# Kernel tuning notes

Hardware: AMD Instinct MI355X
Metric: run time of the kernel (lower is better)

## Reference

```python
import jax, jax.numpy as jnp
import numpy as np

B, N, DM, H = 1, 2048, 1024, 16
CURV = 1.0  # hyperbolic curvature


def setup_inputs() -> dict:
    key = jax.random.key(0)
    ks = jax.random.split(key, 5)
    s = 1.0 / np.sqrt(DM)  # nn.Linear default init scale
    x = jax.random.normal(ks[0], (B, N, DM), dtype=jnp.float32)
    Wq = jax.random.uniform(ks[1], (DM, DM), jnp.float32, -s, s)
    Wk = jax.random.uniform(ks[2], (DM, DM), jnp.float32, -s, s)
    Wv = jax.random.uniform(ks[3], (DM, DM), jnp.float32, -s, s)
    Wo = jax.random.uniform(ks[4], (DM, DM), jnp.float32, -s, s)
    return {"x": x, "Wq": Wq, "Wk": Wk, "Wv": Wv, "Wo": Wo}


def reference(x, Wq, Wk, Wv, Wo):
    b, n, d = x.shape
    hd = d // H

    def split_heads(t):  # [B,N,D] -> [B,H,N,hd]
        return t.reshape(b, n, H, hd).transpose(0, 2, 1, 3)

    q = split_heads(x @ Wq.T)
    k = split_heads(x @ Wk.T)
    v = split_heads(x @ Wv.T)

    q_norm_sq = jnp.sum(q * q, axis=-1, keepdims=True)      # [B,H,N,1]
    k_norm_sq = jnp.sum(k * k, axis=-1)[:, :, None, :]      # [B,H,1,N]
    qk = jnp.einsum('bhnd,bhmd->bhnm', q, k)                # [B,H,N,N]

    diff_sq = jnp.maximum(q_norm_sq + k_norm_sq - 2.0 * qk, 0.0)
    denom = jnp.maximum((1.0 - CURV * q_norm_sq) * (1.0 - CURV * k_norm_sq), 1e-6)
    cosh_arg = jnp.maximum(1.0 + 2.0 * CURV * diff_sq / denom, 1.0)
    # safe acosh: acosh(1)=0; mask avoids inf grad at the boundary
    distance = jnp.where(cosh_arg > 1.0,
                         jnp.arccosh(jnp.maximum(cosh_arg, 1.0 + 1e-12)),
                         0.0)

    attn = jax.nn.softmax(-distance, axis=-1)               # [B,H,N,N]
    out = jnp.einsum('bhnm,bhmd->bhnd', attn, v)            # [B,H,N,hd]
    out = out.transpose(0, 2, 1, 3).reshape(b, n, d)
    return out @ Wo.T
```

## Files before the change

### kernel.cpp

```cpp
#include <hip/hip_runtime.h>
#include <math.h>

#define NSEQ   2048
#define DMODEL 1024
#define NHEADS 16
#define HD     64

typedef short bf16x8 __attribute__((ext_vector_type(8)));
typedef float f32x4  __attribute__((ext_vector_type(4)));
typedef unsigned short ushort8_t __attribute__((ext_vector_type(8)));

__device__ __forceinline__ unsigned short f2bf(float x) {
    unsigned int u = __builtin_bit_cast(unsigned int, x);
    unsigned int r = (u + 0x7FFFu + ((u >> 16) & 1u)) >> 16;
    return (unsigned short)r;
}

__global__ __launch_bounds__(256) void convert_inputs(
    const float* __restrict__ x,  const float* __restrict__ Wq,
    const float* __restrict__ Wk, const float* __restrict__ Wv,
    const float* __restrict__ Wo,
    unsigned short* __restrict__ xb, unsigned short* __restrict__ Wb,
    unsigned short* __restrict__ Wob)
{
    const size_t i8 = ((size_t)blockIdx.x * 256 + threadIdx.x) * 8;
    const float* src;
    unsigned short* dst;
    if (i8 < (2ull << 20)) {
        src = x + i8;  dst = xb + i8;
    } else if (i8 < (5ull << 20)) {
        const size_t o = i8 - (2ull << 20);
        const size_t s = o >> 20;
        src = (s == 0 ? Wq : (s == 1 ? Wk : Wv)) + (o & ((1u << 20) - 1));
        dst = Wb + o;
    } else {
        const size_t o = i8 - (5ull << 20);
        src = Wo + o;  dst = Wob + o;
    }
    const float4 v0 = *reinterpret_cast<const float4*>(src);
    const float4 v1 = *reinterpret_cast<const float4*>(src + 4);
    ushort8_t r;
    r[0] = f2bf(v0.x); r[1] = f2bf(v0.y); r[2] = f2bf(v0.z); r[3] = f2bf(v0.w);
    r[4] = f2bf(v1.x); r[5] = f2bf(v1.y); r[6] = f2bf(v1.z); r[7] = f2bf(v1.w);
    *reinterpret_cast<ushort8_t*>(dst) = r;
}

template <int QKV>
__global__ __launch_bounds__(256) void gemm_bt_bf16(
    const unsigned short* __restrict__ A, const unsigned short* __restrict__ B,
    float* __restrict__ C0,
    unsigned short* __restrict__ QbO, float* __restrict__ qnO,
    float* __restrict__ cq2O,
    unsigned short* __restrict__ KbO, float* __restrict__ knO,
    float* __restrict__ ckO,
    unsigned short* __restrict__ VbO)
{
    __shared__ unsigned short Ahs[128 * 72];
    __shared__ unsigned short Bhs[128 * 72];

    const int bm   = blockIdx.x * 128;
    const int bn   = blockIdx.y * 128;
    const int t    = threadIdx.x;
    const int wid  = t >> 6;
    const int lane = t & 63;
    const int g    = lane >> 4;
    const int r    = lane & 15;
    const int wm   = (wid >> 1) * 64;
    const int wn   = (wid & 1) * 64;

    f32x4 acc[4][4];
#pragma unroll
    for (int i = 0; i < 4; ++i)
#pragma unroll
        for (int j = 0; j < 4; ++j) acc[i][j] = (f32x4){0.f, 0.f, 0.f, 0.f};

    const int srow = t >> 1;
    const int sseg = (t & 1) * 32;

    for (int k0 = 0; k0 < DMODEL; k0 += 64) {
        __syncthreads();
        ushort8_t av[4], bv[4];
#pragma unroll
        for (int c = 0; c < 4; ++c) {
            av[c] = *reinterpret_cast<const ushort8_t*>(
                &A[(size_t)(bm + srow) * DMODEL + k0 + sseg + c * 8]);
            bv[c] = *reinterpret_cast<const ushort8_t*>(
                &B[(size_t)(bn + srow) * DMODEL + k0 + sseg + c * 8]);
        }
#pragma unroll
        for (int c = 0; c < 4; ++c) {
            *reinterpret_cast<ushort8_t*>(&Ahs[srow * 72 + sseg + c * 8]) = av[c];
            *reinterpret_cast<ushort8_t*>(&Bhs[srow * 72 + sseg + c * 8]) = bv[c];
        }
        __syncthreads();

#pragma unroll
        for (int dc = 0; dc < 2; ++dc) {
            bf16x8 af[4], bfr[4];
#pragma unroll
            for (int mt = 0; mt < 4; ++mt)
                af[mt] = *reinterpret_cast<const bf16x8*>(
                    &Ahs[(wm + mt * 16 + r) * 72 + dc * 32 + g * 8]);
#pragma unroll
            for (int nt = 0; nt < 4; ++nt)
                bfr[nt] = *reinterpret_cast<const bf16x8*>(
                    &Bhs[(wn + nt * 16 + r) * 72 + dc * 32 + g * 8]);
#pragma unroll
            for (int mt = 0; mt < 4; ++mt)
#pragma unroll
                for (int nt = 0; nt < 4; ++nt)
                    acc[mt][nt] = __builtin_amdgcn_mfma_f32_16x16x32_bf16(
                        af[mt], bfr[nt], acc[mt][nt], 0, 0, 0);
        }
    }

    if (QKV) {
        const int sel = bn >> 10;
        const int bnl = bn & 1023;
        if (sel < 2) {
            unsigned short* Hb = sel ? KbO : QbO;
            float* narr = sel ? knO : qnO;
            float* carr = sel ? ckO : cq2O;
            const int hh = (bnl + wn) >> 6;
#pragma unroll
            for (int mt = 0; mt < 4; ++mt) {
#pragma unroll
                for (int rg = 0; rg < 4; ++rg) {
                    float ss = 0.f;
#pragma unroll
                    for (int nt = 0; nt < 4; ++nt) {
                        const float v = acc[mt][nt][rg];
                        ss = fmaf(v, v, ss);
                        Hb[(size_t)(bm + wm + mt * 16 + g * 4 + rg) * 1024 +
                           bnl + wn + nt * 16 + r] = f2bf(v);
                    }
                    ss += __shfl_xor(ss, 1, 64);
                    ss += __shfl_xor(ss, 2, 64);
                    ss += __shfl_xor(ss, 4, 64);
                    ss += __shfl_xor(ss, 8, 64);
                    if (r == 0) {
                        const int row = bm + wm + mt * 16 + g * 4 + rg;
                        narr[hh * NSEQ + row] = ss;
                        carr[hh * NSEQ + row] =
                            (sel ? 1.0f : 2.0f) / (1.0f - ss);
                    }
                }
            }
        } else {
#pragma unroll
            for (int mt = 0; mt < 4; ++mt)
#pragma unroll
                for (int nt = 0; nt < 4; ++nt)
#pragma unroll
                    for (int rg = 0; rg < 4; ++rg)
                        VbO[(size_t)(bm + wm + mt * 16 + g * 4 + rg) * 1024 +
                            bnl + wn + nt * 16 + r] = f2bf(acc[mt][nt][rg]);
        }
    } else {
#pragma unroll
        for (int mt = 0; mt < 4; ++mt)
#pragma unroll
            for (int nt = 0; nt < 4; ++nt)
#pragma unroll
                for (int rg = 0; rg < 4; ++rg)
                    C0[(size_t)(bm + wm + mt * 16 + g * 4 + rg) * 1024 +
                       bn + wn + nt * 16 + r] = acc[mt][nt][rg];
    }
}

__global__ __launch_bounds__(256) void vt_kernel_bf16(
    const unsigned short* __restrict__ Vb, unsigned short* __restrict__ Vt)
{
    __shared__ unsigned short Vs[64 * 72];
    const int h   = blockIdx.y;
    const int n0  = blockIdx.x * 64;
    const int t   = threadIdx.x;
    const int row = t >> 2;
    const int seg = (t & 3) * 16;

    const unsigned short* src = Vb + (size_t)(n0 + row) * 1024 + h * HD + seg;
    *reinterpret_cast<ushort8_t*>(&Vs[row * 72 + seg]) =
        *reinterpret_cast<const ushort8_t*>(src);
    *reinterpret_cast<ushort8_t*>(&Vs[row * 72 + seg + 8]) =
        *reinterpret_cast<const ushort8_t*>(src + 8);
    __syncthreads();

    ushort8_t a, b;
#pragma unroll
    for (int c = 0; c < 8; ++c) a[c] = Vs[(seg + c) * 72 + row];
#pragma unroll
    for (int c = 0; c < 8; ++c) b[c] = Vs[(seg + 8 + c) * 72 + row];
    unsigned short* dst = Vt + (size_t)(h * HD + row) * NSEQ + n0 + seg;
    *reinterpret_cast<ushort8_t*>(dst)     = a;
    *reinterpret_cast<ushort8_t*>(dst + 8) = b;
}

__global__ __launch_bounds__(256) void hyp_attn_v3(
    const unsigned short* __restrict__ Qb, const unsigned short* __restrict__ Kb,
    const unsigned short* __restrict__ Vt,
    const float* __restrict__ qn_a, const float* __restrict__ cq2_a,
    const float* __restrict__ kn_a, const float* __restrict__ ck_a,
    float* __restrict__ Opart, float* __restrict__ lpart)
{
    __shared__ unsigned short Khs[64 * 64];
    __shared__ unsigned short Vts[64 * 64];
    __shared__ unsigned short Ps[4][16 * 64];

    const int h    = blockIdx.y;
    const int n0   = blockIdx.x * 64;
    const int jh   = blockIdx.z;
    const int t    = threadIdx.x;
    const int wid  = t >> 6;
    const int lane = t & 63;
    const int g    = lane >> 4;
    const int r    = lane & 15;
    const int qb   = n0 + wid * 16;

    bf16x8 qf[2];
#pragma unroll
    for (int dc = 0; dc < 2; ++dc)
        qf[dc] = *reinterpret_cast<const bf16x8*>(
            Qb + (size_t)(qb + r) * DMODEL + h * HD + dc * 32 + g * 8);

    float qn_r[4], c2q[4];
#pragma unroll
    for (int rg = 0; rg < 4; ++rg) {
        qn_r[rg] = qn_a[h * NSEQ + qb + g * 4 + rg];
        c2q[rg]  = cq2_a[h * NSEQ + qb + g * 4 + rg];
    }

    f32x4 oacc[4];
#pragma unroll
    for (int nt = 0; nt < 4; ++nt) oacc[nt] = (f32x4){0.f, 0.f, 0.f, 0.f};
    float l_acc[4] = {0.f, 0.f, 0.f, 0.f};

    const int srow = t >> 2;
    const int c0   = (t & 3) * 2;
    const int sw0  = (c0 ^ (srow & 7)) * 8;
    const int sw1  = ((c0 + 1) ^ (srow & 7)) * 8;
    const int sg   = (t & 3) * 16;
    unsigned short* Pw = &Ps[wid][0];

    for (int tb = 0; tb < 16; ++tb) {
        const int j0 = jh * 1024 + tb * 64;
        __syncthreads();
        {
            const unsigned short* ks = Kb + (size_t)(j0 + srow) * DMODEL + h * HD + sg;
            const unsigned short* vs = Vt + (size_t)(h * HD + srow) * NSEQ + j0 + sg;
            *reinterpret_cast<ushort8_t*>(&Khs[srow * 64 + sw0]) =
                *reinterpret_cast<const ushort8_t*>(ks);
            *reinterpret_cast<ushort8_t*>(&Khs[srow * 64 + sw1]) =
                *reinterpret_cast<const ushort8_t*>(ks + 8);
            *reinterpret_cast<ushort8_t*>(&Vts[srow * 64 + sw0]) =
                *reinterpret_cast<const ushort8_t*>(vs);
            *reinterpret_cast<ushort8_t*>(&Vts[srow * 64 + sw1]) =
                *reinterpret_cast<const ushort8_t*>(vs + 8);
        }
        __syncthreads();

#pragma unroll
        for (int jt = 0; jt < 4; ++jt) {
            f32x4 sac = (f32x4){0.f, 0.f, 0.f, 0.f};
#pragma unroll
            for (int dc = 0; dc < 2; ++dc) {
                const bf16x8 kb = *reinterpret_cast<const bf16x8*>(
                    &Khs[(jt * 16 + r) * 64 + ((dc * 4 + g) ^ (r & 7)) * 8]);
                sac = __builtin_amdgcn_mfma_f32_16x16x32_bf16(qf[dc], kb, sac, 0, 0, 0);
            }
            const int jj = j0 + jt * 16 + r;
            const float kn_v = kn_a[h * NSEQ + jj];
            const float ck_v = ck_a[h * NSEQ + jj];
#pragma unroll
            for (int rg = 0; rg < 4; ++rg) {
                const float dsq = fmaf(-2.f, sac[rg], qn_r[rg] + kn_v);
                const float ca  = fmaxf(fmaf(dsq, c2q[rg] * ck_v, 1.f), 1.0f);
                const float s2  = fmaf(ca, ca, -1.f);
                const float wj  = ca - __builtin_amdgcn_sqrtf(s2);
                l_acc[rg] += wj;
                const int qrow = g * 4 + rg;
                Pw[qrow * 64 +
                   ((2 * jt + (r >> 3)) ^ (qrow & 7)) * 8 + (r & 7)] = f2bf(wj);
            }
        }

#pragma unroll
        for (int kc = 0; kc < 2; ++kc) {
            const bf16x8 pa = *reinterpret_cast<const bf16x8*>(
                &Pw[r * 64 + ((kc * 4 + g) ^ (r & 7)) * 8]);
#pragma unroll
            for (int nt = 0; nt < 4; ++nt) {
                const bf16x8 vb = *reinterpret_cast<const bf16x8*>(
                    &Vts[(nt * 16 + r) * 64 + ((kc * 4 + g) ^ (r & 7)) * 8]);
                oacc[nt] = __builtin_amdgcn_mfma_f32_16x16x32_bf16(pa, vb, oacc[nt], 0, 0, 0);
            }
        }
    }

#pragma unroll
    for (int rg = 0; rg < 4; ++rg) {
        l_acc[rg] += __shfl_xor(l_acc[rg], 1, 64);
        l_acc[rg] += __shfl_xor(l_acc[rg], 2, 64);
        l_acc[rg] += __shfl_xor(l_acc[rg], 4, 64);
        l_acc[rg] += __shfl_xor(l_acc[rg], 8, 64);
    }

    float* Op = Opart + (size_t)jh * NSEQ * DMODEL;
#pragma unroll
    for (int nt = 0; nt < 4; ++nt)
#pragma unroll
        for (int rg = 0; rg < 4; ++rg)
            Op[(size_t)(qb + g * 4 + rg) * DMODEL + h * HD + nt * 16 + r] =
                oacc[nt][rg];
    if (r == 0) {
#pragma unroll
        for (int rg = 0; rg < 4; ++rg)
            lpart[(jh * NHEADS + h) * NSEQ + qb + g * 4 + rg] = l_acc[rg];
    }
}

__global__ __launch_bounds__(256) void merge_kernel(
    const float* __restrict__ Opart, const float* __restrict__ lpart,
    unsigned short* __restrict__ Ob)
{
    const size_t i8 = ((size_t)blockIdx.x * 256 + threadIdx.x) * 8;
    if (i8 >= (size_t)NSEQ * DMODEL) return;
    const int n  = (int)(i8 >> 10);
    const int dm = (int)(i8 & 1023);
    const int h  = dm >> 6;
    const float li = 1.0f / (lpart[h * NSEQ + n] +
                             lpart[(NHEADS + h) * NSEQ + n]);
    const float* O0 = Opart + i8;
    const float* O1 = Opart + (size_t)NSEQ * DMODEL + i8;
    ushort8_t o;
#pragma unroll
    for (int c = 0; c < 2; ++c) {
        const float4 a = *reinterpret_cast<const float4*>(O0 + c * 4);
        const float4 b = *reinterpret_cast<const float4*>(O1 + c * 4);
        o[c * 4 + 0] = f2bf((a.x + b.x) * li);
        o[c * 4 + 1] = f2bf((a.y + b.y) * li);
        o[c * 4 + 2] = f2bf((a.z + b.z) * li);
        o[c * 4 + 3] = f2bf((a.w + b.w) * li);
    }
    *reinterpret_cast<ushort8_t*>(Ob + i8) = o;
}

extern "C" void kernel_launch(void* const* d_in, const int* in_sizes, int n_in,
                              void* d_out, int out_size, void* d_ws, size_t ws_size,
                              hipStream_t stream)
{
    const float* x  = (const float*)d_in[0];
    const float* Wq = (const float*)d_in[1];
    const float* Wk = (const float*)d_in[2];
    const float* Wv = (const float*)d_in[3];
    const float* Wo = (const float*)d_in[4];
    float* out = (float*)d_out;

    char* ws = (char*)d_ws;
    const size_t MB = 1048576;
    unsigned short* xb   = (unsigned short*)(ws);
    unsigned short* Wb   = (unsigned short*)(ws + 4  * MB);
    unsigned short* Wob  = (unsigned short*)(ws + 10 * MB);
    unsigned short* Qbuf = (unsigned short*)(ws + 12 * MB);
    unsigned short* Kbuf = (unsigned short*)(ws + 16 * MB);
    unsigned short* Vb   = (unsigned short*)(ws + 20 * MB);
    unsigned short* Vt   = (unsigned short*)(ws + 24 * MB);
    float*          qn   = (float*)(ws + 28 * MB);
    float*          cq2  = qn  + NHEADS * NSEQ;
    float*          kn   = cq2 + NHEADS * NSEQ;
    float*          ck   = kn  + NHEADS * NSEQ;
    float*          Opart= (float*)(ws + 29 * MB);
    float*          lpart= (float*)(ws + 45 * MB);
    unsigned short* Ob   = xb;

    const dim3 blk(256);

    convert_inputs<<<3072, blk, 0, stream>>>(x, Wq, Wk, Wv, Wo, xb, Wb, Wob);

    gemm_bt_bf16<1><<<dim3(NSEQ / 128, 3072 / 128), blk, 0, stream>>>(
        xb, Wb, nullptr, Qbuf, qn, cq2, Kbuf, kn, ck, Vb);

    vt_kernel_bf16<<<dim3(NSEQ / 64, NHEADS), blk, 0, stream>>>(Vb, Vt);

    hyp_attn_v3<<<dim3(NSEQ / 64, NHEADS, 2), blk, 0, stream>>>(
        Qbuf, Kbuf, Vt, qn, cq2, kn, ck, Opart, lpart);

    merge_kernel<<<(NSEQ * DMODEL / 8 + 255) / 256, blk, 0, stream>>>(
        Opart, lpart, Ob);

    gemm_bt_bf16<0><<<dim3(NSEQ / 128, DMODEL / 128), blk, 0, stream>>>(
        Ob, Wob, out, nullptr, nullptr, nullptr,
        nullptr, nullptr, nullptr, nullptr);
}
```

Measured before the change: 112.3 us.

## Fuse split-KV merge into output GEMM and transpose score MFMA for packed P stores

Removes the separate merge kernel by having the output projection GEMM read both fp32 partial attention outputs, sum and normalize them by the combined row sums, and convert to bf16 while staging its A tile. The attention kernel swaps the MFMA operands so each lane holds four consecutive keys for one query row. This allows vectorized float4 loads of key norms and packed bf16 stores of P through v_cvt_pk_bf16_f32, and cuts the row-sum reduction to two shuffles. The costs are that the output GEMM now reads fp32 partials (double the bytes) with no load pipelining, and the merge work is repeated across the 8 column blocks.

```diff
diff --git a/kernel.cpp b/kernel.cpp
--- a/kernel.cpp
+++ b/kernel.cpp
@@ -14,6 +14,11 @@
     unsigned int u = __builtin_bit_cast(unsigned int, x);
     unsigned int r = (u + 0x7FFFu + ((u >> 16) & 1u)) >> 16;
     return (unsigned short)r;
+}
+__device__ __forceinline__ unsigned int cvt_pk_bf16(float lo, float hi) {
+    unsigned int d;
+    asm("v_cvt_pk_bf16_f32 %0, %1, %2" : "=v"(d) : "v"(lo), "v"(hi));
+    return d;
 }
 
 __global__ __launch_bounds__(256) void convert_inputs(
@@ -45,10 +50,8 @@
     *reinterpret_cast<ushort8_t*>(dst) = r;
 }
 
-template <int QKV>
-__global__ __launch_bounds__(256) void gemm_bt_bf16(
+__global__ __launch_bounds__(256) void gemm_qkv(
     const unsigned short* __restrict__ A, const unsigned short* __restrict__ B,
-    float* __restrict__ C0,
     unsigned short* __restrict__ QbO, float* __restrict__ qnO,
     float* __restrict__ cq2O,
     unsigned short* __restrict__ KbO, float* __restrict__ knO,
@@ -114,47 +117,35 @@
         }
     }
 
-    if (QKV) {
-        const int sel = bn >> 10;
-        const int bnl = bn & 1023;
-        if (sel < 2) {
-            unsigned short* Hb = sel ? KbO : QbO;
-            float* narr = sel ? knO : qnO;
-            float* carr = sel ? ckO : cq2O;
-            const int hh = (bnl + wn) >> 6;
-#pragma unroll
-            for (int mt = 0; mt < 4; ++mt) {
-#pragma unroll
-                for (int rg = 0; rg < 4; ++rg) {
-                    float ss = 0.f;
-#pragma unroll
-                    for (int nt = 0; nt < 4; ++nt) {
-                        const float v = acc[mt][nt][rg];
-                        ss = fmaf(v, v, ss);
-                        Hb[(size_t)(bm + wm + mt * 16 + g * 4 + rg) * 1024 +
-                           bnl + wn + nt * 16 + r] = f2bf(v);
-                    }
-                    ss += __shfl_xor(ss, 1, 64);
-                    ss += __shfl_xor(ss, 2, 64);
-                    ss += __shfl_xor(ss, 4, 64);
-                    ss += __shfl_xor(ss, 8, 64);
-                    if (r == 0) {
-                        const int row = bm + wm + mt * 16 + g * 4 + rg;
-                        narr[hh * NSEQ + row] = ss;
-                        carr[hh * NSEQ + row] =
-                            (sel ? 1.0f : 2.0f) / (1.0f - ss);
-                    }
+    const int sel = bn >> 10;
+    const int bnl = bn & 1023;
+    if (sel < 2) {
+        unsigned short* Hb = sel ? KbO : QbO;
+        float* narr = sel ? knO : qnO;
+        float* carr = sel ? ckO : cq2O;
+        const int hh = (bnl + wn) >> 6;
+#pragma unroll
+        for (int mt = 0; mt < 4; ++mt) {
+#pragma unroll
+            for (int rg = 0; rg < 4; ++rg) {
+                float ss = 0.f;
+#pragma unroll
+                for (int nt = 0; nt < 4; ++nt) {
+                    const float v = acc[mt][nt][rg];
+                    ss = fmaf(v, v, ss);
+                    Hb[(size_t)(bm + wm + mt * 16 + g * 4 + rg) * 1024 +
+                       bnl + wn + nt * 16 + r] = f2bf(v);
+                }
+                ss += __shfl_xor(ss, 1, 64);
+                ss += __shfl_xor(ss, 2, 64);
+                ss += __shfl_xor(ss, 4, 64);
+                ss += __shfl_xor(ss, 8, 64);
+                if (r == 0) {
+                    const int row = bm + wm + mt * 16 + g * 4 + rg;
+                    narr[hh * NSEQ + row] = ss;
+                    carr[hh * NSEQ + row] = (sel ? 1.0f : 2.0f) / (1.0f - ss);
                 }
             }
-        } else {
-#pragma unroll
-            for (int mt = 0; mt < 4; ++mt)
-#pragma unroll
-                for (int nt = 0; nt < 4; ++nt)
-#pragma unroll
-                    for (int rg = 0; rg < 4; ++rg)
-                        VbO[(size_t)(bm + wm + mt * 16 + g * 4 + rg) * 1024 +
-                            bnl + wn + nt * 16 + r] = f2bf(acc[mt][nt][rg]);
         }
     } else {
 #pragma unroll
@@ -163,8 +154,8 @@
             for (int nt = 0; nt < 4; ++nt)
 #pragma unroll
                 for (int rg = 0; rg < 4; ++rg)
-                    C0[(size_t)(bm + wm + mt * 16 + g * 4 + rg) * 1024 +
-                       bn + wn + nt * 16 + r] = acc[mt][nt][rg];
+                    VbO[(size_t)(bm + wm + mt * 16 + g * 4 + rg) * 1024 +
+                        bnl + wn + nt * 16 + r] = f2bf(acc[mt][nt][rg]);
     }
 }
 
@@ -195,7 +186,7 @@
     *reinterpret_cast<ushort8_t*>(dst + 8) = b;
 }
 
-__global__ __launch_bounds__(256) void hyp_attn_v3(
+__global__ __launch_bounds__(256) void hyp_attn_v4(
     const unsigned short* __restrict__ Qb, const unsigned short* __restrict__ Kb,
     const unsigned short* __restrict__ Vt,
     const float* __restrict__ qn_a, const float* __restrict__ cq2_a,
@@ -222,17 +213,13 @@
         qf[dc] = *reinterpret_cast<const bf16x8*>(
             Qb + (size_t)(qb + r) * DMODEL + h * HD + dc * 32 + g * 8);
 
-    float qn_r[4], c2q[4];
-#pragma unroll
-    for (int rg = 0; rg < 4; ++rg) {
-        qn_r[rg] = qn_a[h * NSEQ + qb + g * 4 + rg];
-        c2q[rg]  = cq2_a[h * NSEQ + qb + g * 4 + rg];
-    }
+    const float qn_l = qn_a[h * NSEQ + qb + r];
+    const float c2q  = cq2_a[h * NSEQ + qb + r];
 
     f32x4 oacc[4];
 #pragma unroll
     for (int nt = 0; nt < 4; ++nt) oacc[nt] = (f32x4){0.f, 0.f, 0.f, 0.f};
-    float l_acc[4] = {0.f, 0.f, 0.f, 0.f};
+    float l_acc = 0.f;
 
     const int srow = t >> 2;
     const int c0   = (t & 3) * 2;
@@ -240,6 +227,7 @@
     const int sw1  = ((c0 + 1) ^ (srow & 7)) * 8;
     const int sg   = (t & 3) * 16;
     unsigned short* Pw = &Ps[wid][0];
+    char* PwB = (char*)Pw + r * 128 + 8 * (g & 1);
 
     for (int tb = 0; tb < 16; ++tb) {
         const int j0 = jh * 1024 + tb * 64;
@@ -265,22 +253,30 @@
             for (int dc = 0; dc < 2; ++dc) {
                 const bf16x8 kb = *reinterpret_cast<const bf16x8*>(
                     &Khs[(jt * 16 + r) * 64 + ((dc * 4 + g) ^ (r & 7)) * 8]);
-                sac = __builtin_amdgcn_mfma_f32_16x16x32_bf16(qf[dc], kb, sac, 0, 0, 0);
+                sac = __builtin_amdgcn_mfma_f32_16x16x32_bf16(kb, qf[dc], sac, 0, 0, 0);
             }
-            const int jj = j0 + jt * 16 + r;
-            const float kn_v = kn_a[h * NSEQ + jj];
-            const float ck_v = ck_a[h * NSEQ + jj];
+            const int jbase = j0 + jt * 16 + g * 4;
+            const float4 kn4 = *reinterpret_cast<const float4*>(
+                &kn_a[h * NSEQ + jbase]);
+            const float4 ck4 = *reinterpret_cast<const float4*>(
+                &ck_a[h * NSEQ + jbase]);
+            const float knv[4] = {kn4.x, kn4.y, kn4.z, kn4.w};
+            const float ckv[4] = {ck4.x, ck4.y, ck4.z, ck4.w};
+            float w[4];
 #pragma unroll
             for (int rg = 0; rg < 4; ++rg) {
-                const float dsq = fmaf(-2.f, sac[rg], qn_r[rg] + kn_v);
-                const float ca  = fmaxf(fmaf(dsq, c2q[rg] * ck_v, 1.f), 1.0f);
+                const float dsq = fmaf(-2.f, sac[rg], qn_l + knv[rg]);
+                const float ca  = fmaxf(fmaf(dsq, c2q * ckv[rg], 1.f), 1.0f);
                 const float s2  = fmaf(ca, ca, -1.f);
                 const float wj  = ca - __builtin_amdgcn_sqrtf(s2);
-                l_acc[rg] += wj;
-                const int qrow = g * 4 + rg;
-                Pw[qrow * 64 +
-                   ((2 * jt + (r >> 3)) ^ (qrow & 7)) * 8 + (r & 7)] = f2bf(wj);
+                l_acc += wj;
+                w[rg] = wj;
             }
+            uint2 pkd;
+            pkd.x = cvt_pk_bf16(w[0], w[1]);
+            pkd.y = cvt_pk_bf16(w[2], w[3]);
+            *reinterpret_cast<uint2*>(
+                PwB + (((2 * jt + (g >> 1)) ^ (r & 7)) << 4)) = pkd;
         }
 
 #pragma unroll
@@ -296,13 +292,8 @@
         }
     }
 
-#pragma unroll
-    for (int rg = 0; rg < 4; ++rg) {
-        l_acc[rg] += __shfl_xor(l_acc[rg], 1, 64);
-        l_acc[rg] += __shfl_xor(l_acc[rg], 2, 64);
-        l_acc[rg] += __shfl_xor(l_acc[rg], 4, 64);
-        l_acc[rg] += __shfl_xor(l_acc[rg], 8, 64);
-    }
+    l_acc += __shfl_xor(l_acc, 16, 64);
+    l_acc += __shfl_xor(l_acc, 32, 64);
 
     float* Op = Opart + (size_t)jh * NSEQ * DMODEL;
 #pragma unroll
@@ -311,37 +302,97 @@
         for (int rg = 0; rg < 4; ++rg)
             Op[(size_t)(qb + g * 4 + rg) * DMODEL + h * HD + nt * 16 + r] =
                 oacc[nt][rg];
-    if (r == 0) {
-#pragma unroll
-        for (int rg = 0; rg < 4; ++rg)
-            lpart[(jh * NHEADS + h) * NSEQ + qb + g * 4 + rg] = l_acc[rg];
+    if (lane < 16)
+        lpart[(jh * NHEADS + h) * NSEQ + qb + r] = l_acc;
+}
+
+__global__ __launch_bounds__(256) void gemm_out_merge(
+    const float* __restrict__ O0, const float* __restrict__ O1,
+    const float* __restrict__ lp,
+    const unsigned short* __restrict__ B,
+    float* __restrict__ C)
+{
+    __shared__ unsigned short Ahs[128 * 72];
+    __shared__ unsigned short Bhs[128 * 72];
+
+    const int bm   = blockIdx.x * 128;
+    const int bn   = blockIdx.y * 128;
+    const int t    = threadIdx.x;
+    const int wid  = t >> 6;
+    const int lane = t & 63;
+    const int g    = lane >> 4;
+    const int r    = lane & 15;
+    const int wm   = (wid >> 1) * 64;
+    const int wn   = (wid & 1) * 64;
+
+    f32x4 acc[4][4];
+#pragma unroll
+    for (int i = 0; i < 4; ++i)
+#pragma unroll
+        for (int j = 0; j < 4; ++j) acc[i][j] = (f32x4){0.f, 0.f, 0.f, 0.f};
+
+    const int srow = t >> 1;
+    const int sseg = (t & 1) * 32;
+    const int arow = bm + srow;
+
+    for (int k0 = 0; k0 < DMODEL; k0 += 64) {
+        __syncthreads();
+        const int hseg = (k0 + sseg) >> 6;
+        const float li = __builtin_amdgcn_rcpf(
+            lp[hseg * NSEQ + arow] + lp[(NHEADS + hseg) * NSEQ + arow]);
+        const float* a0 = &O0[(size_t)arow * DMODEL + k0 + sseg];
+        const float* a1 = &O1[(size_t)arow * DMODEL + k0 + sseg];
+        unsigned int pk8[16];
+#pragma unroll
+        for (int c = 0; c < 8; ++c) {
+            const float4 x0 = *reinterpret_cast<const float4*>(a0 + c * 4);
+            const float4 y0 = *reinterpret_cast<const float4*>(a1 + c * 4);
+            pk8[2 * c]     = cvt_pk_bf16((x0.x + y0.x) * li, (x0.y + y0.y) * li);
+            pk8[2 * c + 1] = cvt_pk_bf16((x0.z + y0.z) * li, (x0.w + y0.w) * li);
+        }
+        ushort8_t bv[4];
+#pragma unroll
+        for (int c = 0; c < 4; ++c)
+            bv[c] = *reinterpret_cast<const ushort8_t*>(
+                &B[(size_t)(bn + srow) * DMODEL + k0 + sseg + c * 8]);
+#pragma unroll
+        for (int c = 0; c < 4; ++c) {
+            uint4 w;
+            w.x = pk8[4 * c]; w.y = pk8[4 * c + 1];
+            w.z = pk8[4 * c + 2]; w.w = pk8[4 * c + 3];
+            *reinterpret_cast<uint4*>(&Ahs[srow * 72 + sseg + c * 8]) = w;
+            *reinterpret_cast<ushort8_t*>(&Bhs[srow * 72 + sseg + c * 8]) = bv[c];
+        }
+        __syncthreads();
+
+#pragma unroll
+        for (int dc = 0; dc < 2; ++dc) {
+            bf16x8 af[4], bfr[4];
+#pragma unroll
+            for (int mt = 0; mt < 4; ++mt)
+                af[mt] = *reinterpret_cast<const bf16x8*>(
+                    &Ahs[(wm + mt * 16 + r) * 72 + dc * 32 + g * 8]);
+#pragma unroll
+            for (int nt = 0; nt < 4; ++nt)
+                bfr[nt] = *reinterpret_cast<const bf16x8*>(
+                    &Bhs[(wn + nt * 16 + r) * 72 + dc * 32 + g * 8]);
+#pragma unroll
+            for (int mt = 0; mt < 4; ++mt)
+#pragma unroll
+                for (int nt = 0; nt < 4; ++nt)
+                    acc[mt][nt] = __builtin_amdgcn_mfma_f32_16x16x32_bf16(
+                        af[mt], bfr[nt], acc[mt][nt], 0, 0, 0);
+        }
     }
-}
-
-__global__ __launch_bounds__(256) void merge_kernel(
-    const float* __restrict__ Opart, const float* __restrict__ lpart,
-    unsigned short* __restrict__ Ob)
-{
-    const size_t i8 = ((size_t)blockIdx.x * 256 + threadIdx.x) * 8;
-    if (i8 >= (size_t)NSEQ * DMODEL) return;
-    const int n  = (int)(i8 >> 10);
-    const int dm = (int)(i8 & 1023);
-    const int h  = dm >> 6;
-    const float li = 1.0f / (lpart[h * NSEQ + n] +
-                             lpart[(NHEADS + h) * NSEQ + n]);
-    const float* O0 = Opart + i8;
-    const float* O1 = Opart + (size_t)NSEQ * DMODEL + i8;
-    ushort8_t o;
-#pragma unroll
-    for (int c = 0; c < 2; ++c) {
-        const float4 a = *reinterpret_cast<const float4*>(O0 + c * 4);
-        const float4 b = *reinterpret_cast<const float4*>(O1 + c * 4);
-        o[c * 4 + 0] = f2bf((a.x + b.x) * li);
-        o[c * 4 + 1] = f2bf((a.y + b.y) * li);
-        o[c * 4 + 2] = f2bf((a.z + b.z) * li);
-        o[c * 4 + 3] = f2bf((a.w + b.w) * li);
-    }
-    *reinterpret_cast<ushort8_t*>(Ob + i8) = o;
+
+#pragma unroll
+    for (int mt = 0; mt < 4; ++mt)
+#pragma unroll
+        for (int nt = 0; nt < 4; ++nt)
+#pragma unroll
+            for (int rg = 0; rg < 4; ++rg)
+                C[(size_t)(bm + wm + mt * 16 + g * 4 + rg) * 1024 +
+                  bn + wn + nt * 16 + r] = acc[mt][nt][rg];
 }
 
 extern "C" void kernel_launch(void* const* d_in, const int* in_sizes, int n_in,
@@ -370,24 +421,19 @@
     float*          ck   = kn  + NHEADS * NSEQ;
     float*          Opart= (float*)(ws + 29 * MB);
     float*          lpart= (float*)(ws + 45 * MB);
-    unsigned short* Ob   = xb;
 
     const dim3 blk(256);
 
     convert_inputs<<<3072, blk, 0, stream>>>(x, Wq, Wk, Wv, Wo, xb, Wb, Wob);
 
-    gemm_bt_bf16<1><<<dim3(NSEQ / 128, 3072 / 128), blk, 0, stream>>>(
-        xb, Wb, nullptr, Qbuf, qn, cq2, Kbuf, kn, ck, Vb);
+    gemm_qkv<<<dim3(NSEQ / 128, 3072 / 128), blk, 0, stream>>>(
+        xb, Wb, Qbuf, qn, cq2, Kbuf, kn, ck, Vb);
 
     vt_kernel_bf16<<<dim3(NSEQ / 64, NHEADS), blk, 0, stream>>>(Vb, Vt);
 
-    hyp_attn_v3<<<dim3(NSEQ / 64, NHEADS, 2), blk, 0, stream>>>(
+    hyp_attn_v4<<<dim3(NSEQ / 64, NHEADS, 2), blk, 0, stream>>>(
         Qbuf, Kbuf, Vt, qn, cq2, kn, ck, Opart, lpart);
 
-    merge_kernel<<<(NSEQ * DMODEL / 8 + 255) / 256, blk, 0, stream>>>(
-        Opart, lpart, Ob);
-
-    gemm_bt_bf16<0><<<dim3(NSEQ / 128, DMODEL / 128), blk, 0, stream>>>(
-        Ob, Wob, out, nullptr, nullptr, nullptr,
-        nullptr, nullptr, nullptr, nullptr);
-}
+    gemm_out_merge<<<dim3(NSEQ / 128, DMODEL / 128), blk, 0, stream>>>(
+        Opart, Opart + (size_t)NSEQ * DMODEL, lpart, Wob, out);
+}
```

Result: slower. 151.5 us (+34.9%).

## Fuse fp32-to-bf16 conversion into GEMM tile loads with XOR-swizzled LDS

Applied to the files above, without the earlier changes.

Removes the separate input conversion kernel. Both GEMMs now read fp32 x and the weights directly and pack them to bf16 with v_cvt_pk_bf16_f32 while staging tiles into shared memory. The shared-memory tiles also switch from padded rows to an XOR swizzle, which shrinks LDS use while still avoiding bank conflicts. The trade-off is that each GEMM block reads twice the global bytes, and inputs are re-read and re-converted once per tile row and column, instead of once up front.

```diff
diff --git a/kernel.cpp b/kernel.cpp
--- a/kernel.cpp
+++ b/kernel.cpp
@@ -15,48 +15,24 @@
     unsigned int r = (u + 0x7FFFu + ((u >> 16) & 1u)) >> 16;
     return (unsigned short)r;
 }
-
-__global__ __launch_bounds__(256) void convert_inputs(
-    const float* __restrict__ x,  const float* __restrict__ Wq,
-    const float* __restrict__ Wk, const float* __restrict__ Wv,
-    const float* __restrict__ Wo,
-    unsigned short* __restrict__ xb, unsigned short* __restrict__ Wb,
-    unsigned short* __restrict__ Wob)
-{
-    const size_t i8 = ((size_t)blockIdx.x * 256 + threadIdx.x) * 8;
-    const float* src;
-    unsigned short* dst;
-    if (i8 < (2ull << 20)) {
-        src = x + i8;  dst = xb + i8;
-    } else if (i8 < (5ull << 20)) {
-        const size_t o = i8 - (2ull << 20);
-        const size_t s = o >> 20;
-        src = (s == 0 ? Wq : (s == 1 ? Wk : Wv)) + (o & ((1u << 20) - 1));
-        dst = Wb + o;
-    } else {
-        const size_t o = i8 - (5ull << 20);
-        src = Wo + o;  dst = Wob + o;
-    }
-    const float4 v0 = *reinterpret_cast<const float4*>(src);
-    const float4 v1 = *reinterpret_cast<const float4*>(src + 4);
-    ushort8_t r;
-    r[0] = f2bf(v0.x); r[1] = f2bf(v0.y); r[2] = f2bf(v0.z); r[3] = f2bf(v0.w);
-    r[4] = f2bf(v1.x); r[5] = f2bf(v1.y); r[6] = f2bf(v1.z); r[7] = f2bf(v1.w);
-    *reinterpret_cast<ushort8_t*>(dst) = r;
-}
-
-template <int QKV>
-__global__ __launch_bounds__(256) void gemm_bt_bf16(
-    const unsigned short* __restrict__ A, const unsigned short* __restrict__ B,
-    float* __restrict__ C0,
+__device__ __forceinline__ unsigned int cvt_pk_bf16(float lo, float hi) {
+    unsigned int d;
+    asm("v_cvt_pk_bf16_f32 %0, %1, %2" : "=v"(d) : "v"(lo), "v"(hi));
+    return d;
+}
+
+__global__ __launch_bounds__(256) void gemm_qkv(
+    const float* __restrict__ X,
+    const float* __restrict__ Wq, const float* __restrict__ Wk,
+    const float* __restrict__ Wv,
     unsigned short* __restrict__ QbO, float* __restrict__ qnO,
     float* __restrict__ cq2O,
     unsigned short* __restrict__ KbO, float* __restrict__ knO,
     float* __restrict__ ckO,
     unsigned short* __restrict__ VbO)
 {
-    __shared__ unsigned short Ahs[128 * 72];
-    __shared__ unsigned short Bhs[128 * 72];
+    __shared__ unsigned short Ahs[128 * 64];
+    __shared__ unsigned short Bhs[128 * 64];
 
     const int bm   = blockIdx.x * 128;
     const int bn   = blockIdx.y * 128;
@@ -68,6 +44,10 @@
     const int wm   = (wid >> 1) * 64;
     const int wn   = (wid & 1) * 64;
 
+    const int sel = bn >> 10;
+    const int bnl = bn & 1023;
+    const float* Bp = (sel == 0) ? Wq : ((sel == 1) ? Wk : Wv);
+
     f32x4 acc[4][4];
 #pragma unroll
     for (int i = 0; i < 4; ++i)
@@ -75,22 +55,33 @@
         for (int j = 0; j < 4; ++j) acc[i][j] = (f32x4){0.f, 0.f, 0.f, 0.f};
 
     const int srow = t >> 1;
-    const int sseg = (t & 1) * 32;
+    const int shal = (t & 1) * 32;
 
     for (int k0 = 0; k0 < DMODEL; k0 += 64) {
         __syncthreads();
-        ushort8_t av[4], bv[4];
+        const float* ag = &X[(size_t)(bm + srow) * DMODEL + k0 + shal];
+        const float* bg = &Bp[(size_t)(bnl + srow) * DMODEL + k0 + shal];
+        unsigned int apk[16], bpk[16];
+#pragma unroll
+        for (int c4 = 0; c4 < 8; ++c4) {
+            const float4 va = *reinterpret_cast<const float4*>(ag + c4 * 4);
+            apk[2 * c4]     = cvt_pk_bf16(va.x, va.y);
+            apk[2 * c4 + 1] = cvt_pk_bf16(va.z, va.w);
+            const float4 vb = *reinterpret_cast<const float4*>(bg + c4 * 4);
+            bpk[2 * c4]     = cvt_pk_bf16(vb.x, vb.y);
+            bpk[2 * c4 + 1] = cvt_pk_bf16(vb.z, vb.w);
+        }
 #pragma unroll
         for (int c = 0; c < 4; ++c) {
-            av[c] = *reinterpret_cast<const ushort8_t*>(
-                &A[(size_t)(bm + srow) * DMODEL + k0 + sseg + c * 8]);
-            bv[c] = *reinterpret_cast<const ushort8_t*>(
-                &B[(size_t)(bn + srow) * DMODEL + k0 + sseg + c * 8]);
-        }
-#pragma unroll
-        for (int c = 0; c < 4; ++c) {
-            *reinterpret_cast<ushort8_t*>(&Ahs[srow * 72 + sseg + c * 8]) = av[c];
-            *reinterpret_cast<ushort8_t*>(&Bhs[srow * 72 + sseg + c * 8]) = bv[c];
+            const int seg = (t & 1) * 4 + c;
+            const int sw  = (seg ^ (srow & 7)) * 8;
+            uint4 wa, wb;
+            wa.x = apk[4 * c]; wa.y = apk[4 * c + 1];
+            wa.z = apk[4 * c + 2]; wa.w = apk[4 * c + 3];
+            wb.x = bpk[4 * c]; wb.y = bpk[4 * c + 1];
+            wb.z = bpk[4 * c + 2]; wb.w = bpk[4 * c + 3];
+            *reinterpret_cast<uint4*>(&Ahs[srow * 64 + sw]) = wa;
+            *reinterpret_cast<uint4*>(&Bhs[srow * 64 + sw]) = wb;
         }
         __syncthreads();
 
@@ -100,11 +91,11 @@
 #pragma unroll
             for (int mt = 0; mt < 4; ++mt)
                 af[mt] = *reinterpret_cast<const bf16x8*>(
-                    &Ahs[(wm + mt * 16 + r) * 72 + dc * 32 + g * 8]);
+                    &Ahs[(wm + mt * 16 + r) * 64 + ((dc * 4 + g) ^ (r & 7)) * 8]);
 #pragma unroll
             for (int nt = 0; nt < 4; ++nt)
                 bfr[nt] = *reinterpret_cast<const bf16x8*>(
-                    &Bhs[(wn + nt * 16 + r) * 72 + dc * 32 + g * 8]);
+                    &Bhs[(wn + nt * 16 + r) * 64 + ((dc * 4 + g) ^ (r & 7)) * 8]);
 #pragma unroll
             for (int mt = 0; mt < 4; ++mt)
 #pragma unroll
@@ -114,47 +105,33 @@
         }
     }
 
-    if (QKV) {
-        const int sel = bn >> 10;
-        const int bnl = bn & 1023;
-        if (sel < 2) {
-            unsigned short* Hb = sel ? KbO : QbO;
-            float* narr = sel ? knO : qnO;
-            float* carr = sel ? ckO : cq2O;
-            const int hh = (bnl + wn) >> 6;
-#pragma unroll
-            for (int mt = 0; mt < 4; ++mt) {
-#pragma unroll
-                for (int rg = 0; rg < 4; ++rg) {
-                    float ss = 0.f;
-#pragma unroll
-                    for (int nt = 0; nt < 4; ++nt) {
-                        const float v = acc[mt][nt][rg];
-                        ss = fmaf(v, v, ss);
-                        Hb[(size_t)(bm + wm + mt * 16 + g * 4 + rg) * 1024 +
-                           bnl + wn + nt * 16 + r] = f2bf(v);
-                    }
-                    ss += __shfl_xor(ss, 1, 64);
-                    ss += __shfl_xor(ss, 2, 64);
-                    ss += __shfl_xor(ss, 4, 64);
-                    ss += __shfl_xor(ss, 8, 64);
-                    if (r == 0) {
-                        const int row = bm + wm + mt * 16 + g * 4 + rg;
-                        narr[hh * NSEQ + row] = ss;
-                        carr[hh * NSEQ + row] =
-                            (sel ? 1.0f : 2.0f) / (1.0f - ss);
-                    }
+    if (sel < 2) {
+        unsigned short* Hb = sel ? KbO : QbO;
+        float* narr = sel ? knO : qnO;
+        float* carr = sel ? ckO : cq2O;
+        const int hh = (bnl + wn) >> 6;
+#pragma unroll
+        for (int mt = 0; mt < 4; ++mt) {
+#pragma unroll
+            for (int rg = 0; rg < 4; ++rg) {
+                float ss = 0.f;
+#pragma unroll
+                for (int nt = 0; nt < 4; ++nt) {
+                    const float v = acc[mt][nt][rg];
+                    ss = fmaf(v, v, ss);
+                    Hb[(size_t)(bm + wm + mt * 16 + g * 4 + rg) * 1024 +
+                       bnl + wn + nt * 16 + r] = f2bf(v);
+                }
+                ss += __shfl_xor(ss, 1, 64);
+                ss += __shfl_xor(ss, 2, 64);
+                ss += __shfl_xor(ss, 4, 64);
+                ss += __shfl_xor(ss, 8, 64);
+                if (r == 0) {
+                    const int row = bm + wm + mt * 16 + g * 4 + rg;
+                    narr[hh * NSEQ + row] = ss;
+                    carr[hh * NSEQ + row] = (sel ? 1.0f : 2.0f) / (1.0f - ss);
                 }
             }
-        } else {
-#pragma unroll
-            for (int mt = 0; mt < 4; ++mt)
-#pragma unroll
-                for (int nt = 0; nt < 4; ++nt)
-#pragma unroll
-                    for (int rg = 0; rg < 4; ++rg)
-                        VbO[(size_t)(bm + wm + mt * 16 + g * 4 + rg) * 1024 +
-                            bnl + wn + nt * 16 + r] = f2bf(acc[mt][nt][rg]);
         }
     } else {
 #pragma unroll
@@ -163,8 +140,8 @@
             for (int nt = 0; nt < 4; ++nt)
 #pragma unroll
                 for (int rg = 0; rg < 4; ++rg)
-                    C0[(size_t)(bm + wm + mt * 16 + g * 4 + rg) * 1024 +
-                       bn + wn + nt * 16 + r] = acc[mt][nt][rg];
+                    VbO[(size_t)(bm + wm + mt * 16 + g * 4 + rg) * 1024 +
+                        bnl + wn + nt * 16 + r] = f2bf(acc[mt][nt][rg]);
     }
 }
 
@@ -344,6 +321,89 @@
     *reinterpret_cast<ushort8_t*>(Ob + i8) = o;
 }
 
+__global__ __launch_bounds__(256) void gemm_out(
+    const unsigned short* __restrict__ A, const float* __restrict__ B,
+    float* __restrict__ C)
+{
+    __shared__ unsigned short Ahs[128 * 64];
+    __shared__ unsigned short Bhs[128 * 64];
+
+    const int bm   = blockIdx.x * 128;
+    const int bn   = blockIdx.y * 128;
+    const int t    = threadIdx.x;
+    const int wid  = t >> 6;
+    const int lane = t & 63;
+    const int g    = lane >> 4;
+    const int r    = lane & 15;
+    const int wm   = (wid >> 1) * 64;
+    const int wn   = (wid & 1) * 64;
+
+    f32x4 acc[4][4];
+#pragma unroll
+    for (int i = 0; i < 4; ++i)
+#pragma unroll
+        for (int j = 0; j < 4; ++j) acc[i][j] = (f32x4){0.f, 0.f, 0.f, 0.f};
+
+    const int srow = t >> 1;
+    const int shal = (t & 1) * 32;
+
+    for (int k0 = 0; k0 < DMODEL; k0 += 64) {
+        __syncthreads();
+        const unsigned short* ag = &A[(size_t)(bm + srow) * DMODEL + k0 + shal];
+        const float* bg = &B[(size_t)(bn + srow) * DMODEL + k0 + shal];
+        ushort8_t av[4];
+        unsigned int bpk[16];
+#pragma unroll
+        for (int c = 0; c < 4; ++c)
+            av[c] = *reinterpret_cast<const ushort8_t*>(ag + c * 8);
+#pragma unroll
+        for (int c4 = 0; c4 < 8; ++c4) {
+            const float4 vb = *reinterpret_cast<const float4*>(bg + c4 * 4);
+            bpk[2 * c4]     = cvt_pk_bf16(vb.x, vb.y);
+            bpk[2 * c4 + 1] = cvt_pk_bf16(vb.z, vb.w);
+        }
+#pragma unroll
+        for (int c = 0; c < 4; ++c) {
+            const int seg = (t & 1) * 4 + c;
+            const int sw  = (seg ^ (srow & 7)) * 8;
+            *reinterpret_cast<ushort8_t*>(&Ahs[srow * 64 + sw]) = av[c];
+            uint4 wb;
+            wb.x = bpk[4 * c]; wb.y = bpk[4 * c + 1];
+            wb.z = bpk[4 * c + 2]; wb.w = bpk[4 * c + 3];
+            *reinterpret_cast<uint4*>(&Bhs[srow * 64 + sw]) = wb;
+        }
+        __syncthreads();
+
+#pragma unroll
+        for (int dc = 0; dc < 2; ++dc) {
+            bf16x8 af[4], bfr[4];
+#pragma unroll
+            for (int mt = 0; mt < 4; ++mt)
+                af[mt] = *reinterpret_cast<const bf16x8*>(
+                    &Ahs[(wm + mt * 16 + r) * 64 + ((dc * 4 + g) ^ (r & 7)) * 8]);
+#pragma unroll
+            for (int nt = 0; nt < 4; ++nt)
+                bfr[nt] = *reinterpret_cast<const bf16x8*>(
+                    &Bhs[(wn + nt * 16 + r) * 64 + ((dc * 4 + g) ^ (r & 7)) * 8]);
+#pragma unroll
+            for (int mt = 0; mt < 4; ++mt)
+#pragma unroll
+                for (int nt = 0; nt < 4; ++nt)
+                    acc[mt][nt] = __builtin_amdgcn_mfma_f32_16x16x32_bf16(
+                        af[mt], bfr[nt], acc[mt][nt], 0, 0, 0);
+        }
+    }
+
+#pragma unroll
+    for (int mt = 0; mt < 4; ++mt)
+#pragma unroll
+        for (int nt = 0; nt < 4; ++nt)
+#pragma unroll
+            for (int rg = 0; rg < 4; ++rg)
+                C[(size_t)(bm + wm + mt * 16 + g * 4 + rg) * 1024 +
+                  bn + wn + nt * 16 + r] = acc[mt][nt][rg];
+}
+
 extern "C" void kernel_launch(void* const* d_in, const int* in_sizes, int n_in,
                               void* d_out, int out_size, void* d_ws, size_t ws_size,
                               hipStream_t stream)
@@ -357,27 +417,22 @@
 
     char* ws = (char*)d_ws;
     const size_t MB = 1048576;
-    unsigned short* xb   = (unsigned short*)(ws);
-    unsigned short* Wb   = (unsigned short*)(ws + 4  * MB);
-    unsigned short* Wob  = (unsigned short*)(ws + 10 * MB);
-    unsigned short* Qbuf = (unsigned short*)(ws + 12 * MB);
-    unsigned short* Kbuf = (unsigned short*)(ws + 16 * MB);
-    unsigned short* Vb   = (unsigned short*)(ws + 20 * MB);
-    unsigned short* Vt   = (unsigned short*)(ws + 24 * MB);
-    float*          qn   = (float*)(ws + 28 * MB);
+    unsigned short* Qbuf = (unsigned short*)(ws);
+    unsigned short* Kbuf = (unsigned short*)(ws + 4  * MB);
+    unsigned short* Vb   = (unsigned short*)(ws + 8  * MB);
+    unsigned short* Vt   = (unsigned short*)(ws + 12 * MB);
+    unsigned short* Ob   = (unsigned short*)(ws + 16 * MB);
+    float*          qn   = (float*)(ws + 20 * MB);
     float*          cq2  = qn  + NHEADS * NSEQ;
     float*          kn   = cq2 + NHEADS * NSEQ;
     float*          ck   = kn  + NHEADS * NSEQ;
-    float*          Opart= (float*)(ws + 29 * MB);
-    float*          lpart= (float*)(ws + 45 * MB);
-    unsigned short* Ob   = xb;
+    float*          Opart= (float*)(ws + 21 * MB);
+    float*          lpart= (float*)(ws + 37 * MB);
 
     const dim3 blk(256);
 
-    convert_inputs<<<3072, blk, 0, stream>>>(x, Wq, Wk, Wv, Wo, xb, Wb, Wob);
-
-    gemm_bt_bf16<1><<<dim3(NSEQ / 128, 3072 / 128), blk, 0, stream>>>(
-        xb, Wb, nullptr, Qbuf, qn, cq2, Kbuf, kn, ck, Vb);
+    gemm_qkv<<<dim3(NSEQ / 128, 3072 / 128), blk, 0, stream>>>(
+        x, Wq, Wk, Wv, Qbuf, qn, cq2, Kbuf, kn, ck, Vb);
 
     vt_kernel_bf16<<<dim3(NSEQ / 64, NHEADS), blk, 0, stream>>>(Vb, Vt);
 
@@ -387,7 +442,6 @@
     merge_kernel<<<(NSEQ * DMODEL / 8 + 255) / 256, blk, 0, stream>>>(
         Opart, lpart, Ob);
 
-    gemm_bt_bf16<0><<<dim3(NSEQ / 128, DMODEL / 128), blk, 0, stream>>>(
-        Ob, Wob, out, nullptr, nullptr, nullptr,
-        nullptr, nullptr, nullptr, nullptr);
-}
+    gemm_out<<<dim3(NSEQ / 128, DMODEL / 128), blk, 0, stream>>>(
+        Ob, Wo, out);
+}
```

New measurement: 167.3 us. +48.9%, slower.
